# Optimization experiments

Measured on AMD Instinct MI355X. Metric: run time of the kernel, lower is better.

## Reference

```python
import jax, jax.numpy as jnp
import numpy as np

B, S, D, H = 2, 2048, 1024, 16
DK = D // H


def setup_inputs() -> dict:
    key = jax.random.key(0)
    ks = jax.random.split(key, 11)
    sc = 0.02
    return {
        "q": jax.random.normal(ks[0], (B, S, D), jnp.float32),
        "k": jax.random.normal(ks[1], (B, S, D), jnp.float32),
        "v": jax.random.normal(ks[2], (B, S, D), jnp.float32),
        "mask": jnp.ones((1, 1, S, S), jnp.int32),
        "w_q": jax.random.normal(ks[3], (D, D), jnp.float32) * sc,
        "b_q": jnp.zeros((D,), jnp.float32),
        "w_k": jax.random.normal(ks[4], (D, D), jnp.float32) * sc,
        "b_k": jnp.zeros((D,), jnp.float32),
        "w_v": jax.random.normal(ks[5], (D, D), jnp.float32) * sc,
        "b_v": jnp.zeros((D,), jnp.float32),
        "w_o": jax.random.normal(ks[6], (D, D), jnp.float32) * sc,
        "b_o": jnp.zeros((D,), jnp.float32),
    }


def reference(q, k, v, mask, w_q, b_q, w_k, b_k, w_v, b_v, w_o, b_o):
    # projections (torch Linear: x @ W.T + b)
    Q = q @ w_q.T + b_q
    K = k @ w_k.T + b_k
    V = v @ w_v.T + b_v
    # [B,S,D] -> [B,H,S,DK]
    Q = Q.reshape(B, S, H, DK).transpose(0, 2, 1, 3)
    K = K.reshape(B, S, H, DK).transpose(0, 2, 1, 3)
    V = V.reshape(B, S, H, DK).transpose(0, 2, 1, 3)
    scores = jnp.einsum('bhqd,bhkd->bhqk', Q, K) / jnp.sqrt(jnp.float32(DK))
    scores = jnp.where(mask == 0, jnp.float32(-1e9), scores)
    attn = jax.nn.softmax(scores, axis=-1)  # dropout p=0.0 -> identity
    X = jnp.einsum('bhqk,bhkd->bhqd', attn, V)
    X = X.transpose(0, 2, 1, 3).reshape(B, S, D)
    return X @ w_o.T + b_o
```

## Files before the change

### kernel.cpp

```cpp
#include <hip/hip_runtime.h>
#include <hip/hip_bf16.h>
#include <cstdint>
#include <cstddef>


typedef __attribute__((ext_vector_type(8))) short short8;
typedef __attribute__((ext_vector_type(4))) float float4v;
typedef __attribute__((ext_vector_type(4))) unsigned short us4;

#define DEV __device__ __forceinline__
#define MFMA16(a, b, c) __builtin_amdgcn_mfma_f32_16x16x32_bf16((a), (b), (c), 0, 0, 0)

DEV unsigned short f2bf(float f) {
  union { float f; unsigned u; } c; c.f = f;
  unsigned u = c.u + 0x7fffu + ((c.u >> 16) & 1u);
  return (unsigned short)(u >> 16);
}

DEV unsigned pkbf2(float a, float b) {
  __hip_bfloat162 h = __float22bfloat162_rn(make_float2(a, b));
  union { __hip_bfloat162 h; unsigned u; } c; c.h = h;
  return c.u;
}

DEV void async16(const void* g, void* l) {
  __builtin_amdgcn_global_load_lds(
      (__attribute__((address_space(1))) void*)(uintptr_t)g,
      (__attribute__((address_space(3))) void*)l, 16, 0, 0);
}

struct CvtJob { const float* src; unsigned short* dst; int n; int mode; };
struct CvtArgs { CvtJob job[8]; };

__global__ __launch_bounds__(256) void cvt_bf16_kernel(CvtArgs args) {
  CvtJob j = args.job[blockIdx.y];
  int i = (blockIdx.x * 256 + threadIdx.x) * 8;
  if (i >= j.n) return;
  if (j.mode == 0) {
    float4v a = *(const float4v*)(j.src + i);
    float4v b = *(const float4v*)(j.src + i + 4);
    short8 o;
#pragma unroll
    for (int t = 0; t < 4; ++t) { o[t] = (short)f2bf(a[t]); o[t + 4] = (short)f2bf(b[t]); }
    *(short8*)(j.dst + i) = o;
  } else {
    const int* mi = (const int*)j.src + i;
    int4 a = ((const int4*)mi)[0], b = ((const int4*)mi)[1];
    unsigned bits = (a.x != 0 ? 1u : 0) | (a.y != 0 ? 2u : 0) | (a.z != 0 ? 4u : 0) |
                    (a.w != 0 ? 8u : 0) | (b.x != 0 ? 16u : 0) | (b.y != 0 ? 32u : 0) |
                    (b.z != 0 ? 64u : 0) | (b.w != 0 ? 128u : 0);
    unsigned long long w = (unsigned long long)bits << ((threadIdx.x & 7) * 8);
    w |= __shfl_xor(w, 1);
    w |= __shfl_xor(w, 2);
    w |= __shfl_xor(w, 4);
    if ((threadIdx.x & 7) == 0) ((unsigned long long*)j.dst)[i >> 6] = w;
  }
}

__global__ __launch_bounds__(64) void mask_flags_kernel(const unsigned long long* __restrict__ mb,
                                                        unsigned int* __restrict__ flags) {
  int qb = blockIdx.x >> 5, kt = blockIdx.x & 31;
  unsigned long long w = mb[(size_t)(qb * 64 + threadIdx.x) * 32 + kt];
  unsigned long long b = __ballot(w == ~0ULL);
  if (threadIdx.x == 0) flags[blockIdx.x] = (b == ~0ULL) ? 1u : 0u;
}

struct GemmJob {
  const unsigned short* A; const unsigned short* W; const float* bias;
  void* out; float scale; int mode;
};
struct GemmArgs { GemmJob job[3]; };

__global__ __launch_bounds__(256, 2) void gemm128_kernel(GemmArgs args) {
  const GemmJob jb = args.job[blockIdx.z];
  const int tid = threadIdx.x;
  const int wave = tid >> 6, lane = tid & 63, lk = lane & 15, quad = lane >> 4;
  const int wm = wave >> 1, wn = wave & 1;
  const int m0 = blockIdx.y * 128, n0 = blockIdx.x * 128;

  __shared__ unsigned short As[128 * 32];
  __shared__ unsigned short Bs[128 * 32];

  float4v acc[4][4] = {};

  const char* Ag = (const char*)jb.A + (size_t)m0 * 2048;
  const char* Wg = (const char*)jb.W + (size_t)n0 * 2048;

#pragma unroll 1
  for (int kk = 0; kk < 32; ++kk) {
    __syncthreads();
    const int kbyte = kk * 64;
#pragma unroll
    for (int i = 0; i < 2; ++i) {
      int o = (wave * 2 + i) * 1024 + lane * 16;
      int r = o >> 6, cb = o & 63;
      async16(Ag + (size_t)r * 2048 + kbyte + cb, (char*)As + (wave * 2 + i) * 1024);
      async16(Wg + (size_t)r * 2048 + kbyte + cb, (char*)Bs + (wave * 2 + i) * 1024);
    }
    __builtin_amdgcn_s_waitcnt(0);
    __syncthreads();

    short8 af[4];
#pragma unroll
    for (int mt = 0; mt < 4; ++mt)
      af[mt] = *(const short8*)(&As[(wm * 64 + mt * 16 + lk) * 32 + quad * 8]);
#pragma unroll
    for (int nt = 0; nt < 4; ++nt) {
      short8 bf = *(const short8*)(&Bs[(wn * 64 + nt * 16 + lk) * 32 + quad * 8]);
#pragma unroll
      for (int mt = 0; mt < 4; ++mt)
        acc[mt][nt] = MFMA16(af[mt], bf, acc[mt][nt]);
    }
  }

  if (jb.mode == 0) {
    unsigned short* outp = (unsigned short*)jb.out;
#pragma unroll
    for (int nt = 0; nt < 4; ++nt) {
      int n = n0 + wn * 64 + nt * 16 + lk;
      float bn = jb.bias[n];
      int h = n >> 6, d = n & 63;
#pragma unroll
      for (int mt = 0; mt < 4; ++mt) {
#pragma unroll
        for (int r = 0; r < 4; ++r) {
          int m = m0 + wm * 64 + mt * 16 + quad * 4 + r;
          int b = m >> 11, s = m & 2047;
          float v = (acc[mt][nt][r] + bn) * jb.scale;
          outp[((size_t)((b * 16 + h) * 2048 + s) << 6) + d] = f2bf(v);
        }
      }
    }
  } else {
    unsigned short* outp = (unsigned short*)jb.out;
#pragma unroll
    for (int nt = 0; nt < 4; ++nt) {
      int n = n0 + wn * 64 + nt * 16 + lk;
      float bn = jb.bias[n];
      int h = n >> 6, d = n & 63;
#pragma unroll
      for (int mt = 0; mt < 4; ++mt) {
        int m = m0 + wm * 64 + mt * 16 + quad * 4;
        int b = m >> 11, s = m & 2047;
        us4 pk;
#pragma unroll
        for (int r = 0; r < 4; ++r) pk[r] = f2bf(acc[mt][nt][r] + bn);
        *(us4*)(&outp[((size_t)((b * 16 + h) * 64 + d) << 11) + s]) = pk;
      }
    }
  }
}

__global__ __launch_bounds__(256, 2) void gemm_out64_kernel(
    const unsigned short* __restrict__ A, const unsigned short* __restrict__ W,
    const float* __restrict__ bias, float* __restrict__ out) {
  const int tid = threadIdx.x;
  const int wave = tid >> 6, lane = tid & 63, lk = lane & 15, quad = lane >> 4;
  const int wm = wave >> 1, wn = wave & 1;
  const int m0 = blockIdx.y * 64, n0 = blockIdx.x * 128;

  __shared__ unsigned short As[64 * 32];
  __shared__ unsigned short Bs[128 * 32];

  float4v acc[2][4] = {};

  const char* Ag = (const char*)A + (size_t)m0 * 2048;
  const char* Wg = (const char*)W + (size_t)n0 * 2048;

#pragma unroll 1
  for (int kk = 0; kk < 32; ++kk) {
    __syncthreads();
    const int kbyte = kk * 64;
    {
      int o = wave * 1024 + lane * 16;
      int r = o >> 6, cb = o & 63;
      async16(Ag + (size_t)r * 2048 + kbyte + cb, (char*)As + wave * 1024);
    }
#pragma unroll
    for (int i = 0; i < 2; ++i) {
      int o = (wave * 2 + i) * 1024 + lane * 16;
      int r = o >> 6, cb = o & 63;
      async16(Wg + (size_t)r * 2048 + kbyte + cb, (char*)Bs + (wave * 2 + i) * 1024);
    }
    __builtin_amdgcn_s_waitcnt(0);
    __syncthreads();

    short8 af[2];
#pragma unroll
    for (int mt = 0; mt < 2; ++mt)
      af[mt] = *(const short8*)(&As[(wm * 32 + mt * 16 + lk) * 32 + quad * 8]);
#pragma unroll
    for (int nt = 0; nt < 4; ++nt) {
      short8 bf = *(const short8*)(&Bs[(wn * 64 + nt * 16 + lk) * 32 + quad * 8]);
#pragma unroll
      for (int mt = 0; mt < 2; ++mt)
        acc[mt][nt] = MFMA16(af[mt], bf, acc[mt][nt]);
    }
  }

#pragma unroll
  for (int nt = 0; nt < 4; ++nt) {
    int n = n0 + wn * 64 + nt * 16 + lk;
    float bn = bias[n];
#pragma unroll
    for (int mt = 0; mt < 2; ++mt) {
#pragma unroll
      for (int r = 0; r < 4; ++r) {
        int m = m0 + wm * 32 + mt * 16 + quad * 4 + r;
        out[(size_t)m * 1024 + n] = acc[mt][nt][r] + bn;
      }
    }
  }
}

__global__ __launch_bounds__(256, 4) void attn_kernel(
    const unsigned short* __restrict__ Qp, const unsigned short* __restrict__ Kp,
    const unsigned short* __restrict__ Vtp, const unsigned int* __restrict__ flags,
    const unsigned long long* __restrict__ mbits, unsigned short* __restrict__ Xout) {
  __shared__ unsigned short Qs[64 * 64];
  __shared__ unsigned short Ks[64 * 64];
  __shared__ unsigned short Vts[64 * 64];
  __shared__ unsigned short Ps[64 * 72];

  const int tid = threadIdx.x, wave = tid >> 6, lane = tid & 63;
  const int lk = lane & 15, quad = lane >> 4;

  const int bid = blockIdx.y * 32 + blockIdx.x;
  const int xcd = bid & 7, idx = bid >> 3;
  const int bh = xcd * 4 + (idx >> 5);
  const int qb = idx & 31, q0 = qb * 64;
  const size_t cbase = (size_t)bh * (2048 * 64);
  const int r8 = lane >> 3, gs = lane & 7;
  const int sw = lk & 7;

#pragma unroll
  for (int i = 0; i < 2; ++i) {
    int row = wave * 16 + i * 8 + r8;
    int g = gs ^ (row & 7);
    async16(Qp + cbase + (size_t)(q0 + row) * 64 + g * 8,
            (char*)Qs + (wave * 16 + i * 8) * 128);
  }
  __builtin_amdgcn_s_waitcnt(0x0f70);

  short8 qf[2];
#pragma unroll
  for (int ks = 0; ks < 2; ++ks) {
    int row = wave * 16 + lk;
    int gg = (ks * 4 + quad) ^ (row & 7);
    qf[ks] = *(const short8*)(&Qs[row * 64 + gg * 8]);
  }

  float rsum = 0.f;
  float4v O[4] = {};

#pragma unroll 1
  for (int kt = 0; kt < 32; ++kt) {
    __syncthreads();
#pragma unroll
    for (int i = 0; i < 2; ++i) {
      int row = wave * 16 + i * 8 + r8;
      int g = gs ^ (row & 7);
      async16(Kp + cbase + (size_t)(kt * 64 + row) * 64 + g * 8,
              (char*)Ks + (wave * 16 + i * 8) * 128);
      async16(Vtp + cbase + (size_t)row * 2048 + kt * 64 + g * 8,
              (char*)Vts + (wave * 16 + i * 8) * 128);
    }
    __builtin_amdgcn_s_waitcnt(0x0f70);
    __syncthreads();

    float4v sacc[4] = {};
#pragma unroll
    for (int kt4 = 0; kt4 < 4; ++kt4) {
      int krow = kt4 * 16 + lk;
      short8 ka0 = *(const short8*)(&Ks[krow * 64 + ((quad) ^ sw) * 8]);
      short8 ka1 = *(const short8*)(&Ks[krow * 64 + ((4 + quad) ^ sw) * 8]);
      sacc[kt4] = MFMA16(ka0, qf[0], sacc[kt4]);
      sacc[kt4] = MFMA16(ka1, qf[1], sacc[kt4]);
    }

    if (__builtin_expect(flags[qb * 32 + kt] == 0, 0)) {
      unsigned long long w = mbits[(size_t)(q0 + wave * 16 + lk) * 32 + kt];
#pragma unroll
      for (int kt4 = 0; kt4 < 4; ++kt4)
#pragma unroll
        for (int r = 0; r < 4; ++r)
          if (!((w >> (kt4 * 16 + quad * 4 + r)) & 1ULL))
            sacc[kt4][r] = -__builtin_inff();
    }

#pragma unroll
    for (int kt4 = 0; kt4 < 4; ++kt4) {
      float p0 = __builtin_amdgcn_exp2f(sacc[kt4][0]);
      float p1 = __builtin_amdgcn_exp2f(sacc[kt4][1]);
      float p2 = __builtin_amdgcn_exp2f(sacc[kt4][2]);
      float p3 = __builtin_amdgcn_exp2f(sacc[kt4][3]);
      rsum += (p0 + p1) + (p2 + p3);
      uint2 pk;
      pk.x = pkbf2(p0, p1);
      pk.y = pkbf2(p2, p3);
      *(uint2*)(&Ps[(wave * 16 + lk) * 72 + kt4 * 16 + quad * 4]) = pk;
    }

    short8 pa[2];
#pragma unroll
    for (int ks = 0; ks < 2; ++ks)
      pa[ks] = *(const short8*)(&Ps[(wave * 16 + lk) * 72 + ks * 32 + quad * 8]);
#pragma unroll
    for (int dt = 0; dt < 4; ++dt) {
      int drow = dt * 16 + lk;
      short8 vb0 = *(const short8*)(&Vts[drow * 64 + ((quad) ^ sw) * 8]);
      short8 vb1 = *(const short8*)(&Vts[drow * 64 + ((4 + quad) ^ sw) * 8]);
      O[dt] = MFMA16(pa[0], vb0, O[dt]);
      O[dt] = MFMA16(pa[1], vb1, O[dt]);
    }
  }

  float s = rsum;
  s += __shfl_xor(s, 16);
  s += __shfl_xor(s, 32);
  float inv = 1.f / s;
  float linv[4];
#pragma unroll
  for (int r = 0; r < 4; ++r) linv[r] = __shfl(inv, quad * 4 + r);

  const int b = bh >> 4, h = bh & 15;
#pragma unroll
  for (int dt = 0; dt < 4; ++dt)
#pragma unroll
    for (int r = 0; r < 4; ++r) {
      int qq = q0 + wave * 16 + quad * 4 + r;
      int d = dt * 16 + lk;
      Xout[((size_t)(b * 2048 + qq)) * 1024 + h * 64 + d] = f2bf(O[dt][r] * linv[r]);
    }
}

extern "C" void kernel_launch(void* const* d_in, const int* in_sizes, int n_in,
                              void* d_out, int out_size, void* d_ws, size_t ws_size,
                              hipStream_t stream) {
  const float* q   = (const float*)d_in[0];
  const float* k   = (const float*)d_in[1];
  const float* v   = (const float*)d_in[2];
  const int*   msk = (const int*)d_in[3];
  const float* w_q = (const float*)d_in[4];
  const float* b_q = (const float*)d_in[5];
  const float* w_k = (const float*)d_in[6];
  const float* b_k = (const float*)d_in[7];
  const float* w_v = (const float*)d_in[8];
  const float* b_v = (const float*)d_in[9];
  const float* w_o = (const float*)d_in[10];
  const float* b_o = (const float*)d_in[11];

  char* ws = (char*)d_ws;
  const size_t MB = (size_t)1 << 20;
  unsigned short* q_bf  = (unsigned short*)(ws + 0 * MB);
  unsigned short* k_bf  = (unsigned short*)(ws + 8 * MB);
  unsigned short* v_bf  = (unsigned short*)(ws + 16 * MB);
  unsigned short* wq_bf = (unsigned short*)(ws + 24 * MB);
  unsigned short* wk_bf = (unsigned short*)(ws + 26 * MB);
  unsigned short* wv_bf = (unsigned short*)(ws + 28 * MB);
  unsigned short* wo_bf = (unsigned short*)(ws + 30 * MB);
  unsigned short* Qp    = (unsigned short*)(ws + 32 * MB);
  unsigned short* Kp    = (unsigned short*)(ws + 40 * MB);
  unsigned short* Vtp   = (unsigned short*)(ws + 48 * MB);
  unsigned short* Xa    = (unsigned short*)(ws + 56 * MB);
  unsigned long long* mb = (unsigned long long*)(ws + 64 * MB);
  unsigned int* mflags   = (unsigned int*)(ws + 64 * MB + (512 << 10));

  CvtArgs ca;
  ca.job[0] = { q,   q_bf,  4096 * 1024, 0 };
  ca.job[1] = { k,   k_bf,  4096 * 1024, 0 };
  ca.job[2] = { v,   v_bf,  4096 * 1024, 0 };
  ca.job[3] = { w_q, wq_bf, 1024 * 1024, 0 };
  ca.job[4] = { w_k, wk_bf, 1024 * 1024, 0 };
  ca.job[5] = { w_v, wv_bf, 1024 * 1024, 0 };
  ca.job[6] = { w_o, wo_bf, 1024 * 1024, 0 };
  ca.job[7] = { (const float*)msk, (unsigned short*)mb, 2048 * 2048, 1 };
  cvt_bf16_kernel<<<dim3(2048, 8), 256, 0, stream>>>(ca);

  mask_flags_kernel<<<dim3(1024), 64, 0, stream>>>(mb, mflags);

  GemmArgs ga;
  ga.job[0] = { q_bf, wq_bf, b_q, (void*)Qp,  0.1803368801111204f, 0 };
  ga.job[1] = { k_bf, wk_bf, b_k, (void*)Kp,  1.0f,   0 };
  ga.job[2] = { v_bf, wv_bf, b_v, (void*)Vtp, 1.0f,   2 };
  gemm128_kernel<<<dim3(8, 32, 3), 256, 0, stream>>>(ga);

  attn_kernel<<<dim3(32, 32), 256, 0, stream>>>(Qp, Kp, Vtp, mflags, mb, Xa);

  gemm_out64_kernel<<<dim3(8, 64), 256, 0, stream>>>(Xa, wo_bf, b_o, (float*)d_out);
}
```

Baseline: 244.5 us.

## Switch projection GEMMs to 32x32 MFMA with swizzled LDS; load Q directly

Both projection GEMM kernels move from 16x16x32 to 32x32x16 bf16 MFMA tiles, with an XOR swizzle on the LDS layout to cut bank conflicts. Occupancy hints are raised (3 and 4 blocks per CU). The attention kernel now loads its Q fragments straight from global memory into registers, dropping the Qs shared buffer and its async copy. The aim is fewer LDS reads per MFMA, less LDS pressure and higher occupancy; the epilogue stores follow the new 32x32 accumulator layout, which risks less coalesced writes.

```diff
diff --git a/kernel.cpp b/kernel.cpp
--- a/kernel.cpp
+++ b/kernel.cpp
@@ -6,10 +6,12 @@
 
 typedef __attribute__((ext_vector_type(8))) short short8;
 typedef __attribute__((ext_vector_type(4))) float float4v;
+typedef __attribute__((ext_vector_type(16))) float float16v;
 typedef __attribute__((ext_vector_type(4))) unsigned short us4;
 
 #define DEV __device__ __forceinline__
 #define MFMA16(a, b, c) __builtin_amdgcn_mfma_f32_16x16x32_bf16((a), (b), (c), 0, 0, 0)
+#define MFMA32(a, b, c) __builtin_amdgcn_mfma_f32_32x32x16_bf16((a), (b), (c), 0, 0, 0)
 
 DEV unsigned short f2bf(float f) {
   union { float f; unsigned u; } c; c.f = f;
@@ -71,17 +73,18 @@
 };
 struct GemmArgs { GemmJob job[3]; };
 
-__global__ __launch_bounds__(256, 2) void gemm128_kernel(GemmArgs args) {
+__global__ __launch_bounds__(256, 3) void gemm128_kernel(GemmArgs args) {
   const GemmJob jb = args.job[blockIdx.z];
   const int tid = threadIdx.x;
-  const int wave = tid >> 6, lane = tid & 63, lk = lane & 15, quad = lane >> 4;
+  const int wave = tid >> 6, lane = tid & 63;
+  const int ln = lane & 31, kh = lane >> 5;
   const int wm = wave >> 1, wn = wave & 1;
   const int m0 = blockIdx.y * 128, n0 = blockIdx.x * 128;
 
   __shared__ unsigned short As[128 * 32];
   __shared__ unsigned short Bs[128 * 32];
 
-  float4v acc[4][4] = {};
+  float16v acc[2][2] = {};
 
   const char* Ag = (const char*)jb.A + (size_t)m0 * 2048;
   const char* Wg = (const char*)jb.W + (size_t)n0 * 2048;
@@ -93,40 +96,51 @@
 #pragma unroll
     for (int i = 0; i < 2; ++i) {
       int o = (wave * 2 + i) * 1024 + lane * 16;
-      int r = o >> 6, cb = o & 63;
+      int r = o >> 6;
+      int g = (o >> 4) & 3;
+      int cb = ((g ^ (r & 3)) << 4);
       async16(Ag + (size_t)r * 2048 + kbyte + cb, (char*)As + (wave * 2 + i) * 1024);
       async16(Wg + (size_t)r * 2048 + kbyte + cb, (char*)Bs + (wave * 2 + i) * 1024);
     }
     __builtin_amdgcn_s_waitcnt(0);
     __syncthreads();
 
-    short8 af[4];
-#pragma unroll
-    for (int mt = 0; mt < 4; ++mt)
-      af[mt] = *(const short8*)(&As[(wm * 64 + mt * 16 + lk) * 32 + quad * 8]);
-#pragma unroll
-    for (int nt = 0; nt < 4; ++nt) {
-      short8 bf = *(const short8*)(&Bs[(wn * 64 + nt * 16 + lk) * 32 + quad * 8]);
-#pragma unroll
-      for (int mt = 0; mt < 4; ++mt)
-        acc[mt][nt] = MFMA16(af[mt], bf, acc[mt][nt]);
+    short8 af[2][2];
+#pragma unroll
+    for (int mt = 0; mt < 2; ++mt)
+#pragma unroll
+      for (int ks = 0; ks < 2; ++ks) {
+        int r = wm * 64 + mt * 32 + ln;
+        int gw = (ks * 2 + kh) ^ (r & 3);
+        af[mt][ks] = *(const short8*)(&As[r * 32 + gw * 8]);
+      }
+#pragma unroll
+    for (int nt = 0; nt < 2; ++nt) {
+      int r = wn * 64 + nt * 32 + ln;
+      short8 bf0 = *(const short8*)(&Bs[r * 32 + ((kh ^ (r & 3)) * 8)]);
+      short8 bf1 = *(const short8*)(&Bs[r * 32 + (((2 + kh) ^ (r & 3)) * 8)]);
+#pragma unroll
+      for (int mt = 0; mt < 2; ++mt) {
+        acc[mt][nt] = MFMA32(af[mt][0], bf0, acc[mt][nt]);
+        acc[mt][nt] = MFMA32(af[mt][1], bf1, acc[mt][nt]);
+      }
     }
   }
 
   if (jb.mode == 0) {
     unsigned short* outp = (unsigned short*)jb.out;
 #pragma unroll
-    for (int nt = 0; nt < 4; ++nt) {
-      int n = n0 + wn * 64 + nt * 16 + lk;
+    for (int nt = 0; nt < 2; ++nt) {
+      int n = n0 + wn * 64 + nt * 32 + ln;
       float bn = jb.bias[n];
       int h = n >> 6, d = n & 63;
 #pragma unroll
-      for (int mt = 0; mt < 4; ++mt) {
-#pragma unroll
-        for (int r = 0; r < 4; ++r) {
-          int m = m0 + wm * 64 + mt * 16 + quad * 4 + r;
+      for (int mt = 0; mt < 2; ++mt) {
+#pragma unroll
+        for (int rg = 0; rg < 16; ++rg) {
+          int m = m0 + wm * 64 + mt * 32 + (rg & 3) + 8 * (rg >> 2) + 4 * kh;
           int b = m >> 11, s = m & 2047;
-          float v = (acc[mt][nt][r] + bn) * jb.scale;
+          float v = (acc[mt][nt][rg] + bn) * jb.scale;
           outp[((size_t)((b * 16 + h) * 2048 + s) << 6) + d] = f2bf(v);
         }
       }
@@ -134,35 +148,39 @@
   } else {
     unsigned short* outp = (unsigned short*)jb.out;
 #pragma unroll
-    for (int nt = 0; nt < 4; ++nt) {
-      int n = n0 + wn * 64 + nt * 16 + lk;
+    for (int nt = 0; nt < 2; ++nt) {
+      int n = n0 + wn * 64 + nt * 32 + ln;
       float bn = jb.bias[n];
       int h = n >> 6, d = n & 63;
 #pragma unroll
-      for (int mt = 0; mt < 4; ++mt) {
-        int m = m0 + wm * 64 + mt * 16 + quad * 4;
-        int b = m >> 11, s = m & 2047;
-        us4 pk;
-#pragma unroll
-        for (int r = 0; r < 4; ++r) pk[r] = f2bf(acc[mt][nt][r] + bn);
-        *(us4*)(&outp[((size_t)((b * 16 + h) * 64 + d) << 11) + s]) = pk;
+      for (int mt = 0; mt < 2; ++mt) {
+#pragma unroll
+        for (int g2 = 0; g2 < 4; ++g2) {
+          int m = m0 + wm * 64 + mt * 32 + 8 * g2 + 4 * kh;
+          int b = m >> 11, s = m & 2047;
+          us4 pk;
+#pragma unroll
+          for (int r = 0; r < 4; ++r) pk[r] = f2bf(acc[mt][nt][g2 * 4 + r] + bn);
+          *(us4*)(&outp[((size_t)((b * 16 + h) * 64 + d) << 11) + s]) = pk;
+        }
       }
     }
   }
 }
 
-__global__ __launch_bounds__(256, 2) void gemm_out64_kernel(
+__global__ __launch_bounds__(256, 4) void gemm_out64_kernel(
     const unsigned short* __restrict__ A, const unsigned short* __restrict__ W,
     const float* __restrict__ bias, float* __restrict__ out) {
   const int tid = threadIdx.x;
-  const int wave = tid >> 6, lane = tid & 63, lk = lane & 15, quad = lane >> 4;
+  const int wave = tid >> 6, lane = tid & 63;
+  const int ln = lane & 31, kh = lane >> 5;
   const int wm = wave >> 1, wn = wave & 1;
   const int m0 = blockIdx.y * 64, n0 = blockIdx.x * 128;
 
   __shared__ unsigned short As[64 * 32];
   __shared__ unsigned short Bs[128 * 32];
 
-  float4v acc[2][4] = {};
+  float16v acc[2] = {};
 
   const char* Ag = (const char*)A + (size_t)m0 * 2048;
   const char* Wg = (const char*)W + (size_t)n0 * 2048;
@@ -173,42 +191,42 @@
     const int kbyte = kk * 64;
     {
       int o = wave * 1024 + lane * 16;
-      int r = o >> 6, cb = o & 63;
+      int r = o >> 6, g = (o >> 4) & 3, cb = ((g ^ (r & 3)) << 4);
       async16(Ag + (size_t)r * 2048 + kbyte + cb, (char*)As + wave * 1024);
     }
 #pragma unroll
     for (int i = 0; i < 2; ++i) {
       int o = (wave * 2 + i) * 1024 + lane * 16;
-      int r = o >> 6, cb = o & 63;
+      int r = o >> 6, g = (o >> 4) & 3, cb = ((g ^ (r & 3)) << 4);
       async16(Wg + (size_t)r * 2048 + kbyte + cb, (char*)Bs + (wave * 2 + i) * 1024);
     }
     __builtin_amdgcn_s_waitcnt(0);
     __syncthreads();
 
-    short8 af[2];
-#pragma unroll
-    for (int mt = 0; mt < 2; ++mt)
-      af[mt] = *(const short8*)(&As[(wm * 32 + mt * 16 + lk) * 32 + quad * 8]);
-#pragma unroll
-    for (int nt = 0; nt < 4; ++nt) {
-      short8 bf = *(const short8*)(&Bs[(wn * 64 + nt * 16 + lk) * 32 + quad * 8]);
-#pragma unroll
-      for (int mt = 0; mt < 2; ++mt)
-        acc[mt][nt] = MFMA16(af[mt], bf, acc[mt][nt]);
-    }
-  }
-
-#pragma unroll
-  for (int nt = 0; nt < 4; ++nt) {
-    int n = n0 + wn * 64 + nt * 16 + lk;
+    short8 af0, af1;
+    {
+      int r = wm * 32 + ln;
+      af0 = *(const short8*)(&As[r * 32 + ((kh ^ (r & 3)) * 8)]);
+      af1 = *(const short8*)(&As[r * 32 + (((2 + kh) ^ (r & 3)) * 8)]);
+    }
+#pragma unroll
+    for (int nt = 0; nt < 2; ++nt) {
+      int r = wn * 64 + nt * 32 + ln;
+      short8 bf0 = *(const short8*)(&Bs[r * 32 + ((kh ^ (r & 3)) * 8)]);
+      short8 bf1 = *(const short8*)(&Bs[r * 32 + (((2 + kh) ^ (r & 3)) * 8)]);
+      acc[nt] = MFMA32(af0, bf0, acc[nt]);
+      acc[nt] = MFMA32(af1, bf1, acc[nt]);
+    }
+  }
+
+#pragma unroll
+  for (int nt = 0; nt < 2; ++nt) {
+    int n = n0 + wn * 64 + nt * 32 + ln;
     float bn = bias[n];
 #pragma unroll
-    for (int mt = 0; mt < 2; ++mt) {
-#pragma unroll
-      for (int r = 0; r < 4; ++r) {
-        int m = m0 + wm * 32 + mt * 16 + quad * 4 + r;
-        out[(size_t)m * 1024 + n] = acc[mt][nt][r] + bn;
-      }
+    for (int rg = 0; rg < 16; ++rg) {
+      int m = m0 + wm * 32 + (rg & 3) + 8 * (rg >> 2) + 4 * kh;
+      out[(size_t)m * 1024 + n] = acc[nt][rg] + bn;
     }
   }
 }
@@ -217,7 +235,6 @@
     const unsigned short* __restrict__ Qp, const unsigned short* __restrict__ Kp,
     const unsigned short* __restrict__ Vtp, const unsigned int* __restrict__ flags,
     const unsigned long long* __restrict__ mbits, unsigned short* __restrict__ Xout) {
-  __shared__ unsigned short Qs[64 * 64];
   __shared__ unsigned short Ks[64 * 64];
   __shared__ unsigned short Vts[64 * 64];
   __shared__ unsigned short Ps[64 * 72];
@@ -233,22 +250,10 @@
   const int r8 = lane >> 3, gs = lane & 7;
   const int sw = lk & 7;
 
-#pragma unroll
-  for (int i = 0; i < 2; ++i) {
-    int row = wave * 16 + i * 8 + r8;
-    int g = gs ^ (row & 7);
-    async16(Qp + cbase + (size_t)(q0 + row) * 64 + g * 8,
-            (char*)Qs + (wave * 16 + i * 8) * 128);
-  }
-  __builtin_amdgcn_s_waitcnt(0x0f70);
-
+  const unsigned short* qrow = Qp + cbase + (size_t)(q0 + wave * 16 + lk) * 64 + quad * 8;
   short8 qf[2];
-#pragma unroll
-  for (int ks = 0; ks < 2; ++ks) {
-    int row = wave * 16 + lk;
-    int gg = (ks * 4 + quad) ^ (row & 7);
-    qf[ks] = *(const short8*)(&Qs[row * 64 + gg * 8]);
-  }
+  qf[0] = *(const short8*)(qrow);
+  qf[1] = *(const short8*)(qrow + 32);
 
   float rsum = 0.f;
   float4v O[4] = {};
```

Result: slower. 252.9 us (+3.4%).
